# Optimization experiments

Hardware: AMD Instinct MI355X
Metric: run time of the kernel (lower is better)

## Reference

```python
import jax, jax.numpy as jnp
import numpy as np

B, S, DIM = 8, 1024, 192
D2 = 2 * DIM            # inner width 384
CH = 4                  # cell heads (= qk_size)
HD = D2 // CH           # 96 head dim
NB = D2 // 4            # 96 block-diagonal blocks
BLK = D2 // NB          # block size 4
TAU = float(HD) ** 0.5


def setup_inputs() -> dict:
    key = jax.random.key(0)
    ks = jax.random.split(key, 16)
    r = lambda i, shp, s=0.02: jax.random.normal(ks[i], shp, jnp.float32) * s
    return {
        "x": jax.random.normal(ks[0], (B, S, DIM), jnp.float32),
        "ln_g": jnp.ones((DIM,), jnp.float32), "ln_b": jnp.zeros((DIM,), jnp.float32),
        "w1": r(1, (D2, DIM)), "b1": jnp.zeros((D2,), jnp.float32),
        "w2": r(2, (D2, DIM)), "b2": jnp.zeros((D2,), jnp.float32),
        "conv_w": r(3, (D2, 1, 3), 0.1), "conv_b": jnp.zeros((D2,), jnp.float32),
        "qw": r(4, (NB, BLK, BLK), 0.1), "qb": jnp.zeros((D2,), jnp.float32),
        "kw": r(5, (NB, BLK, BLK), 0.1), "kb": jnp.zeros((D2,), jnp.float32),
        "vw": r(6, (NB, BLK, BLK), 0.1), "vb": jnp.zeros((D2,), jnp.float32),
        "wi": r(7, (CH, 3 * D2)), "bi": jax.random.normal(ks[8], (CH,), jnp.float32) * 0.1,
        "wf": r(9, (CH, 3 * D2)), "bf": jnp.linspace(3.0, 6.0, CH).astype(jnp.float32),
        "gn_g": jnp.ones((D2,), jnp.float32), "gn_b": jnp.zeros((D2,), jnp.float32),
        "wo": r(10, (DIM, D2)), "bo": jnp.zeros((DIM,), jnp.float32),
        "skip": jnp.ones((D2,), jnp.float32),
    }


def _layernorm(x, g, b):
    m = x.mean(-1, keepdims=True)
    v = ((x - m) ** 2).mean(-1, keepdims=True)
    return (x - m) / jnp.sqrt(v + 1e-5) * g + b


def _blockdiag(x, w, b):
    # x: [B,S,D2] -> blocks [B,S,NB,BLK]; w: [NB, out_blk, in_blk]
    bs, sq, _ = x.shape
    y = jnp.einsum('bsni,noi->bsno', x.reshape(bs, sq, NB, BLK), w)
    return y.reshape(bs, sq, D2) + b


def _dwconv(x, w, b):
    # depthwise conv over sequence: x [B,S,C] -> [B,C,S] conv -> [B,S,C]
    y = jax.lax.conv_general_dilated(
        x.transpose(0, 2, 1), w, window_strides=(1,), padding=[(1, 1)],
        dimension_numbers=('NCH', 'OIH', 'NCH'), feature_group_count=D2)
    return y.transpose(0, 2, 1) + b


def _cell(q, k, v, wi, bi, wf, bf, gn_g, gn_b):
    bs, sq, _ = q.shape
    gi = jnp.concatenate([q, k, v], axis=-1)                      # [B,S,3*D2]
    it = jnp.einsum('bsc,hc->bhs', gi, wi) + bi[None, :, None]    # [B,H,S]
    ft = jnp.einsum('bsc,hc->bhs', gi, wf) + bf[None, :, None]
    c = jnp.cumsum(jax.nn.log_sigmoid(ft), axis=-1)               # [B,H,S]
    logm = c[..., :, None] - c[..., None, :]                      # cum[i]-cum[j]
    mask = jnp.tril(jnp.ones((sq, sq), dtype=bool))
    f_act = jnp.where(mask, logm, -jnp.inf)
    dt = f_act + it[:, :, None, :]                                # add itilde over cols
    max_d = jnp.max(dt, axis=-1, keepdims=True)
    dmat = jnp.exp(dt - max_d)                                    # [B,H,S,S]
    qh = q.reshape(bs, sq, CH, HD).transpose(0, 2, 1, 3)
    kh = k.reshape(bs, sq, CH, HD).transpose(0, 2, 1, 3)
    vh = v.reshape(bs, sq, CH, HD).transpose(0, 2, 1, 3)
    ct = jnp.einsum('bhid,bhjd->bhij', qh, kh) * dmat / TAU
    maxit = jnp.maximum(jnp.abs(ct.sum(-1, keepdims=True)), jnp.exp(-max_d))
    h = jnp.einsum('bhij,bhjd->bhid', ct, vh) / (maxit + 1e-6)
    h = h.transpose(0, 2, 1, 3).reshape(bs, sq, CH, HD)           # per-token GroupNorm
    mu = h.mean(-1, keepdims=True)
    var = ((h - mu) ** 2).mean(-1, keepdims=True)
    h = (h - mu) / jnp.sqrt(var + 1e-5)
    h = h * gn_g.reshape(CH, HD) + gn_b.reshape(CH, HD)
    return h.reshape(bs, sq, D2)


def reference(x, ln_g, ln_b, w1, b1, w2, b2, conv_w, conv_b, qw, qb, kw, kb,
              vw, vb, wi, bi, wf, bf, gn_g, gn_b, wo, bo, skip):
    inputs = _layernorm(x, ln_g, ln_b)
    a = inputs @ w1.T + b1                   # [B,S,D2]
    bgate = jax.nn.silu(inputs @ w2.T + b2)  # [B,S,D2]
    qk = jax.nn.silu(_dwconv(a, conv_w, conv_b))
    q = _blockdiag(qk, qw, qb)
    k = _blockdiag(qk, kw, kb)
    v = _blockdiag(a, vw, vb)
    out1 = _cell(q, k, v, wi, bi, wf, bf, gn_g, gn_b)
    out1 = (out1 + skip * qk) * bgate
    out = out1 @ wo.T + bo
    return out + x
```

## Files before the change

kernel.cpp:

```cpp
#include <hip/hip_runtime.h>
#include <cstdint>

#define TAU_ 9.797958971132712f

typedef __attribute__((ext_vector_type(4))) float f32x4;
typedef __attribute__((ext_vector_type(8))) short short8;

#define DEV static __device__ __forceinline__

DEV unsigned short f2bf(float f){
  union { float f; unsigned u; } v; v.f = f;
  unsigned r = v.u + 0x7FFFu + ((v.u >> 16) & 1u);
  return (unsigned short)(r >> 16);
}
DEV float bf2f(unsigned short u){
  union { unsigned u; float f; } v; v.u = ((unsigned)u) << 16; return v.f;
}
DEV unsigned pack2bf(float a, float b){
  unsigned r;
  asm("v_cvt_pk_bf16_f32 %0, %1, %2" : "=v"(r) : "v"(a), "v"(b));
  return r;
}
DEV f32x4 ld_bf4(const unsigned short* p){
  uint2 r = *(const uint2*)p;
  f32x4 o;
  o[0] = bf2f((unsigned short)(r.x & 0xffff));
  o[1] = bf2f((unsigned short)(r.x >> 16));
  o[2] = bf2f((unsigned short)(r.y & 0xffff));
  o[3] = bf2f((unsigned short)(r.y >> 16));
  return o;
}
DEV float siluf_(float x){ return x / (1.f + __expf(-x)); }
DEV float logsigf_(float x){ return fminf(x, 0.f) - log1pf(__expf(-fabsf(x))); }

__global__ __launch_bounds__(256) void k1a_ln(
    const float* __restrict__ x, const float* __restrict__ ln_g, const float* __restrict__ ln_b,
    const float* __restrict__ w1, const float* __restrict__ w2, const float* __restrict__ wo,
    short* __restrict__ xnbf, short* __restrict__ w12bf, short* __restrict__ wobf)
{
  const int tid = threadIdx.x;
  if(blockIdx.x >= 512){
    const int idx4 = (blockIdx.x - 512) * 256 + tid;
    const float* src; short* dst; int off;
    if(idx4 < 18432)      { src = w1; dst = w12bf;         off = idx4; }
    else if(idx4 < 36864) { src = w2; dst = w12bf + 73728; off = idx4 - 18432; }
    else                  { src = wo; dst = wobf;          off = idx4 - 36864; }
    f32x4 v = *(const f32x4*)(src + off * 4);
    uint2 pk; pk.x = pack2bf(v[0], v[1]); pk.y = pack2bf(v[2], v[3]);
    *(uint2*)(dst + off * 4) = pk;
    return;
  }
  const int t = blockIdx.x * 16 + (tid >> 4);
  const int g = tid & 15;
  const float* xr = x + (long)t * 192 + g * 12;
  f32x4 v0 = *(const f32x4*)(xr);
  f32x4 v1 = *(const f32x4*)(xr + 4);
  f32x4 v2 = *(const f32x4*)(xr + 8);
  float s  = v0[0]+v0[1]+v0[2]+v0[3] + v1[0]+v1[1]+v1[2]+v1[3] + v2[0]+v2[1]+v2[2]+v2[3];
  float sq = v0[0]*v0[0]+v0[1]*v0[1]+v0[2]*v0[2]+v0[3]*v0[3]
           + v1[0]*v1[0]+v1[1]*v1[1]+v1[2]*v1[2]+v1[3]*v1[3]
           + v2[0]*v2[0]+v2[1]*v2[1]+v2[2]*v2[2]+v2[3]*v2[3];
  s  += __shfl_xor(s, 1);  s  += __shfl_xor(s, 2);  s  += __shfl_xor(s, 4);  s  += __shfl_xor(s, 8);
  sq += __shfl_xor(sq, 1); sq += __shfl_xor(sq, 2); sq += __shfl_xor(sq, 4); sq += __shfl_xor(sq, 8);
  const float mean = s * (1.f/192.f);
  const float rstd = rsqrtf(sq * (1.f/192.f) - mean * mean + 1e-5f);
  const int c0 = g * 12;
  f32x4 g0 = *(const f32x4*)(ln_g + c0),     b0 = *(const f32x4*)(ln_b + c0);
  f32x4 g1 = *(const f32x4*)(ln_g + c0 + 4), b1 = *(const f32x4*)(ln_b + c0 + 4);
  f32x4 g2 = *(const f32x4*)(ln_g + c0 + 8), b2 = *(const f32x4*)(ln_b + c0 + 8);
  unsigned pk[6];
  pk[0] = pack2bf((v0[0]-mean)*rstd*g0[0]+b0[0], (v0[1]-mean)*rstd*g0[1]+b0[1]);
  pk[1] = pack2bf((v0[2]-mean)*rstd*g0[2]+b0[2], (v0[3]-mean)*rstd*g0[3]+b0[3]);
  pk[2] = pack2bf((v1[0]-mean)*rstd*g1[0]+b1[0], (v1[1]-mean)*rstd*g1[1]+b1[1]);
  pk[3] = pack2bf((v1[2]-mean)*rstd*g1[2]+b1[2], (v1[3]-mean)*rstd*g1[3]+b1[3]);
  pk[4] = pack2bf((v2[0]-mean)*rstd*g2[0]+b2[0], (v2[1]-mean)*rstd*g2[1]+b2[1]);
  pk[5] = pack2bf((v2[2]-mean)*rstd*g2[2]+b2[2], (v2[3]-mean)*rstd*g2[3]+b2[3]);
  uint2* xo = (uint2*)(xnbf + (long)t * 192 + g * 12);
  xo[0] = make_uint2(pk[0], pk[1]);
  xo[1] = make_uint2(pk[2], pk[3]);
  xo[2] = make_uint2(pk[4], pk[5]);
}

__global__ __launch_bounds__(256) void k1b_gemm(
    const short* __restrict__ xnbf, const short* __restrict__ w12bf,
    const float* __restrict__ b1, const float* __restrict__ b2,
    unsigned short* __restrict__ abf, unsigned short* __restrict__ bgate)
{
  __shared__ short wt[18432];
  const int tid = threadIdx.x;
  const int ntg = blockIdx.x & 7;
  const int t0 = (blockIdx.x >> 3) * 128;
  {
    const short* src = w12bf + (long)ntg * 96 * 192;
    #pragma unroll
    for(int i = 0; i < 9; i++){
      const int u = i * 256 + tid;
      const int row = u / 24;
      const int dst = (u * 16) ^ ((row & 7) << 4);
      *(short8*)((char*)wt + dst) = *(const short8*)(src + u * 8);
    }
  }
  __syncthreads();
  const int widx = tid >> 6, lane = tid & 63, qg = lane >> 4, l16 = lane & 15;
  const int m0 = t0 + widx * 32;
  f32x4 acc[2][6];
  #pragma unroll
  for(int mt = 0; mt < 2; mt++)
    #pragma unroll
    for(int nt = 0; nt < 6; nt++) acc[mt][nt] = (f32x4){0.f,0.f,0.f,0.f};
  const short* xrow0 = xnbf + (long)(m0 + l16) * 192;
  const short* xrow1 = xnbf + (long)(m0 + 16 + l16) * 192;
  #pragma unroll
  for(int kc = 0; kc < 6; kc++){
    short8 af0 = *(const short8*)(xrow0 + kc * 32 + 8 * qg);
    short8 af1 = *(const short8*)(xrow1 + kc * 32 + 8 * qg);
    #pragma unroll
    for(int nt = 0; nt < 6; nt++){
      const int row = nt * 16 + l16;
      int byte = row * 384 + (kc * 32 + 8 * qg) * 2;
      byte ^= (row & 7) << 4;
      short8 bfr = *(const short8*)((const char*)wt + byte);
      acc[0][nt] = __builtin_amdgcn_mfma_f32_16x16x32_bf16(af0, bfr, acc[0][nt], 0, 0, 0);
      acc[1][nt] = __builtin_amdgcn_mfma_f32_16x16x32_bf16(af1, bfr, acc[1][nt], 0, 0, 0);
    }
  }
  const int half = ntg >> 2;
  const float* bias = half ? b2 : b1;
  const int ncol = (ntg & 3) * 96;
  #pragma unroll
  for(int mt = 0; mt < 2; mt++){
    #pragma unroll
    for(int nt = 0; nt < 6; nt++){
      const int n = ncol + nt * 16 + l16;
      const float bs = bias[n];
      #pragma unroll
      for(int r = 0; r < 4; r++){
        const int trow = m0 + mt * 16 + 4 * qg + r;
        float v = acc[mt][nt][r] + bs;
        if(half) bgate[(long)trow * 384 + n] = f2bf(siluf_(v));
        else     abf[(long)trow * 384 + n] = f2bf(v);
      }
    }
  }
}

__global__ __launch_bounds__(256) void k2bv(
    const unsigned short* __restrict__ abf,
    const float* __restrict__ cw, const float* __restrict__ cb,
    const float* __restrict__ qw, const float* __restrict__ qb,
    const float* __restrict__ kw, const float* __restrict__ kb,
    const float* __restrict__ vw, const float* __restrict__ vb,
    unsigned short* __restrict__ qkbf, short* __restrict__ qbf, short* __restrict__ kbf,
    short* __restrict__ vbf, short* __restrict__ vtbf)
{
  __shared__ float vt[64][97];
  const int tid = threadIdx.x;
  const int bh = blockIdx.x >> 4;
  const int b = bh >> 2, h = bh & 3;
  const int s0 = (blockIdx.x & 15) << 6;
  #pragma unroll
  for(int it = 0; it < 6; it++){
    const int f = it * 256 + tid;
    const int sl = f / 24, c4l = f % 24;
    const int c4 = h * 24 + c4l;
    const int s = s0 + sl;
    const long t = (long)b * 1024 + s;
    const long abase = t * 384 + c4 * 4;
    f32x4 am = ld_bf4(abf + abase);
    f32x4 al = (s > 0)    ? ld_bf4(abf + abase - 384) : (f32x4){0.f,0.f,0.f,0.f};
    f32x4 ar = (s < 1023) ? ld_bf4(abf + abase + 384) : (f32x4){0.f,0.f,0.f,0.f};
    f32x4 cw0 = *(const f32x4*)(cw + c4 * 12);
    f32x4 cw1 = *(const f32x4*)(cw + c4 * 12 + 4);
    f32x4 cw2 = *(const f32x4*)(cw + c4 * 12 + 8);
    f32x4 cb4 = *(const f32x4*)(cb + c4 * 4);
    f32x4 in;
    in[0] = siluf_(cb4[0] + al[0]*cw0[0] + am[0]*cw0[1] + ar[0]*cw0[2]);
    in[1] = siluf_(cb4[1] + al[1]*cw0[3] + am[1]*cw1[0] + ar[1]*cw1[1]);
    in[2] = siluf_(cb4[2] + al[2]*cw1[2] + am[2]*cw1[3] + ar[2]*cw2[0]);
    in[3] = siluf_(cb4[3] + al[3]*cw2[1] + am[3]*cw2[2] + ar[3]*cw2[3]);
    {
      uint2 pk; pk.x = pack2bf(in[0], in[1]); pk.y = pack2bf(in[2], in[3]);
      *(uint2*)(qkbf + abase) = pk;
    }
    const long base = ((long)(b * 4 + h) * 1024 + s) * 96 + c4l * 4;
    {
      const float* w = qw + c4 * 16;
      float v0 = qb[c4*4+0] + w[0]*in[0]  + w[1]*in[1]  + w[2]*in[2]  + w[3]*in[3];
      float v1 = qb[c4*4+1] + w[4]*in[0]  + w[5]*in[1]  + w[6]*in[2]  + w[7]*in[3];
      float v2 = qb[c4*4+2] + w[8]*in[0]  + w[9]*in[1]  + w[10]*in[2] + w[11]*in[3];
      float v3 = qb[c4*4+3] + w[12]*in[0] + w[13]*in[1] + w[14]*in[2] + w[15]*in[3];
      uint2 pk; pk.x = pack2bf(v0, v1); pk.y = pack2bf(v2, v3);
      *(uint2*)(qbf + base) = pk;
    }
    {
      const float* w = kw + c4 * 16;
      float v0 = kb[c4*4+0] + w[0]*in[0]  + w[1]*in[1]  + w[2]*in[2]  + w[3]*in[3];
      float v1 = kb[c4*4+1] + w[4]*in[0]  + w[5]*in[1]  + w[6]*in[2]  + w[7]*in[3];
      float v2 = kb[c4*4+2] + w[8]*in[0]  + w[9]*in[1]  + w[10]*in[2] + w[11]*in[3];
      float v3 = kb[c4*4+3] + w[12]*in[0] + w[13]*in[1] + w[14]*in[2] + w[15]*in[3];
      uint2 pk; pk.x = pack2bf(v0, v1); pk.y = pack2bf(v2, v3);
      *(uint2*)(kbf + base) = pk;
    }
    {
      const float* w = vw + c4 * 16;
      float vv[4];
      #pragma unroll
      for(int o = 0; o < 4; o++){
        float v = vb[c4*4+o] + w[o*4]*am[0] + w[o*4+1]*am[1] + w[o*4+2]*am[2] + w[o*4+3]*am[3];
        vv[o] = v;
        vt[sl][c4l * 4 + o] = v;
      }
      uint2 pk; pk.x = pack2bf(vv[0], vv[1]); pk.y = pack2bf(vv[2], vv[3]);
      *(uint2*)(vbf + abase) = pk;
    }
  }
  __syncthreads();
  #pragma unroll
  for(int it = 0; it < 24; it++){
    const int f = it * 256 + tid;
    const int d = f >> 6, sl = f & 63;
    vtbf[((long)bh * 96 + d) * 1024 + s0 + sl] = (short)f2bf(vt[sl][d]);
  }
}

__global__ __launch_bounds__(256) void k2c_gates(
    const short* __restrict__ qbf, const short* __restrict__ kbf, const short* __restrict__ vbf,
    const float* __restrict__ wi, const float* __restrict__ bi,
    const float* __restrict__ wf, const float* __restrict__ bff,
    float* __restrict__ itv, float* __restrict__ ftv)
{
  __shared__ short wg[8 * 1160];
  const int tid = threadIdx.x;
  const int t0 = blockIdx.x * 64;
  #pragma unroll
  for(int i = 0; i < 9; i++){
    const int u = i * 256 + tid;
    const int row = u / 288, col4 = u % 288;
    const float* src = ((row < 4) ? wi + row * 1152 : wf + (row - 4) * 1152) + col4 * 4;
    f32x4 v = *(const f32x4*)src;
    uint2 pk; pk.x = pack2bf(v[0], v[1]); pk.y = pack2bf(v[2], v[3]);
    *(uint2*)(&wg[row * 1160 + col4 * 4]) = pk;
  }
  __syncthreads();
  const int w = tid >> 6, lane = tid & 63, qg = lane >> 4, l16 = lane & 15;
  const int tw = t0 + w * 16;
  const int tA = tw + l16;
  const int b = tA >> 10, s = tA & 1023;
  f32x4 acc = (f32x4){0.f,0.f,0.f,0.f};
  #pragma unroll
  for(int kc = 0; kc < 36; kc++){
    const int blk = kc / 3;
    const int off = (kc % 3) * 32 + qg * 8;
    short8 af;
    if(blk < 4)      af = *(const short8*)(qbf + ((long)(b*4+blk)*1024 + s)*96 + off);
    else if(blk < 8) af = *(const short8*)(kbf + ((long)(b*4+blk-4)*1024 + s)*96 + off);
    else             af = *(const short8*)(vbf + (long)tA*384 + (blk-8)*96 + off);
    short8 bf8 = *(const short8*)(&wg[(l16 & 7) * 1160 + kc * 32 + qg * 8]);
    acc = __builtin_amdgcn_mfma_f32_16x16x32_bf16(af, bf8, acc, 0, 0, 0);
  }
  if(l16 < 8){
    const int gh = l16 & 3;
    const float bias = (l16 < 4) ? bi[gh] : bff[gh];
    float* dst = (l16 < 4) ? itv : ftv;
    #pragma unroll
    for(int r = 0; r < 4; r++){
      const int t = tw + 4 * qg + r;
      dst[((long)((t >> 10) * 4 + gh)) * 1024 + (t & 1023)] = acc[r] + bias;
    }
  }
}

__global__ __launch_bounds__(256) void k3_scan(
    const float* __restrict__ itv, const float* __restrict__ ftv,
    float* __restrict__ Ev, float* __restrict__ Rpv, float* __restrict__ dsv)
{
  __shared__ float sb[256];
  const int bh = blockIdx.x, tid = threadIdx.x;
  const long base = (long)bh * 1024 + tid * 4;
  f32x4 f4 = *(const f32x4*)(ftv + base);
  const float l0 = logsigf_(f4[0]);
  const float l1 = logsigf_(f4[1]);
  const float l2 = logsigf_(f4[2]);
  const float l3 = logsigf_(f4[3]);
  float c0 = l0, c1 = l0 + l1, c2 = c1 + l2, c3 = c2 + l3;
  sb[tid] = c3;
  __syncthreads();
  for(int off = 1; off < 256; off <<= 1){
    float mine = sb[tid];
    float oth = (tid >= off) ? sb[tid - off] : 0.f;
    __syncthreads();
    sb[tid] = mine + oth;
    __syncthreads();
  }
  const float excl = (tid > 0) ? sb[tid - 1] : 0.f;
  c0 += excl; c1 += excl; c2 += excl; c3 += excl;
  f32x4 i4 = *(const f32x4*)(itv + base);
  const float m0 = i4[0] - c0, m1 = i4[1] - c1, m2 = i4[2] - c2, m3 = i4[3] - c3;
  const float x1 = fmaxf(m0, m1), x2 = fmaxf(x1, m2), x3 = fmaxf(x2, m3);
  __syncthreads();
  sb[tid] = x3;
  __syncthreads();
  for(int off = 1; off < 256; off <<= 1){
    float mine = sb[tid];
    float oth = (tid >= off) ? sb[tid - off] : -3.4e38f;
    __syncthreads();
    sb[tid] = fmaxf(mine, oth);
    __syncthreads();
  }
  const float exm = (tid > 0) ? sb[tid - 1] : -3.4e38f;
  const float M0 = fmaxf(m0, exm);
  const float M1 = fmaxf(x1, exm);
  const float M2 = fmaxf(x2, exm);
  const float M3 = fmaxf(x3, exm);
  f32x4 e, rp, ds;
  e[0] = __expf(m0); e[1] = __expf(m1); e[2] = __expf(m2); e[3] = __expf(m3);
  rp[0] = __expf(-M0) * (1.f/TAU_); rp[1] = __expf(-M1) * (1.f/TAU_);
  rp[2] = __expf(-M2) * (1.f/TAU_); rp[3] = __expf(-M3) * (1.f/TAU_);
  ds[0] = __expf(-(c0 + M0)); ds[1] = __expf(-(c1 + M1));
  ds[2] = __expf(-(c2 + M2)); ds[3] = __expf(-(c3 + M3));
  *(f32x4*)(Ev  + base) = e;
  *(f32x4*)(Rpv + base) = rp;
  *(f32x4*)(dsv + base) = ds;
}

__global__ __launch_bounds__(256, 2) void k4_attn(
    const short* __restrict__ qbf, const short* __restrict__ kbf, const short* __restrict__ vtbf,
    const float* __restrict__ Ev, const float* __restrict__ Rpv, const float* __restrict__ dsv,
    const float* __restrict__ gn_g, const float* __restrict__ gn_b,
    const unsigned short* __restrict__ qkbf, const unsigned short* __restrict__ bgate,
    const float* __restrict__ skip, short* __restrict__ o1bf)
{
  __shared__ short kbuf[2][64 * 104];
  __shared__ short vbuf[2][96 * 72];
  __shared__ float ebuf[2][64];
  __shared__ short P[4][16][72];
  const int tid = threadIdx.x;
  const int w = tid >> 6, lane = tid & 63, qg = lane >> 4, l16 = lane & 15;
  const int xcd = blockIdx.x & 7, q = blockIdx.x >> 3;
  const int bh = ((q & 3) << 3) | xcd;
  const int qh = q >> 2;
  const int ib = (q < 32) ? (15 - qh) : (qh - 8);
  const int i0w = ib * 64 + w * 16;
  const long qkbase = (long)bh * 1024;
  const int nj = ib + 1;

  short8 qf[3];
  #pragma unroll
  for(int kc = 0; kc < 3; kc++)
    qf[kc] = *(const short8*)(qbf + (qkbase + i0w + l16) * 96 + kc * 32 + 8 * qg);
  const float rp = Rpv[qkbase + i0w + l16];
  const float ds = dsv[qkbase + i0w + l16];

  f32x4 acc[6];
  #pragma unroll
  for(int dt = 0; dt < 6; dt++) acc[dt] = (f32x4){0.f,0.f,0.f,0.f};
  float bp = 0.f;

  const int rK0 = tid / 12,        cK0 = tid % 12;
  const int rK1 = (tid+256) / 12,  cK1 = (tid+256) % 12;
  const int rK2 = (tid+512) / 12,  cK2 = (tid+512) % 12;
  const int dV0 = tid >> 3,        cV0 = tid & 7;
  const int dV1 = (tid+256) >> 3,  cV1 = (tid+256) & 7;
  const int dV2 = (tid+512) >> 3,  cV2 = (tid+512) & 7;
  const bool he = (tid < 16);
  short8 sk0, sk1, sk2, sv0, sv1, sv2; f32x4 se;
  const short* kgb = kbf + qkbase * 96;
  const short* vgb = vtbf + (long)bh * 96 * 1024;

#define STAGE_LOAD(J0)                                              \
  {                                                                 \
    const int j0_ = (J0);                                           \
    sk0 = *(const short8*)(kgb + (j0_ + rK0) * 96 + cK0 * 8);       \
    sk1 = *(const short8*)(kgb + (j0_ + rK1) * 96 + cK1 * 8);       \
    sk2 = *(const short8*)(kgb + (j0_ + rK2) * 96 + cK2 * 8);       \
    sv0 = *(const short8*)(vgb + (long)dV0 * 1024 + j0_ + cV0 * 8); \
    sv1 = *(const short8*)(vgb + (long)dV1 * 1024 + j0_ + cV1 * 8); \
    sv2 = *(const short8*)(vgb + (long)dV2 * 1024 + j0_ + cV2 * 8); \
    if(he) se = *(const f32x4*)(Ev + qkbase + j0_ + tid * 4);       \
  }

#define STAGE_WRITE(B)                                   \
  {                                                      \
    *(short8*)(&kbuf[B][rK0 * 104 + cK0 * 8]) = sk0;     \
    *(short8*)(&kbuf[B][rK1 * 104 + cK1 * 8]) = sk1;     \
    *(short8*)(&kbuf[B][rK2 * 104 + cK2 * 8]) = sk2;     \
    *(short8*)(&vbuf[B][dV0 * 72 + cV0 * 8]) = sv0;      \
    *(short8*)(&vbuf[B][dV1 * 72 + cV1 * 8]) = sv1;      \
    *(short8*)(&vbuf[B][dV2 * 72 + cV2 * 8]) = sv2;      \
    if(he) *(f32x4*)(&ebuf[B][tid * 4]) = se;            \
  }

  STAGE_LOAD(0);
  int cur = 0;
  for(int jt = 0; jt < nj; jt++){
    STAGE_WRITE(cur);
    __syncthreads();
    if(jt + 1 < nj) STAGE_LOAD((jt + 1) * 64);

    const int j0 = jt * 64;
    const bool diag = (jt == nj - 1);
    const int i = i0w + l16;
    __builtin_amdgcn_s_setprio(1);
    #pragma unroll
    for(int jsub = 0; jsub < 4; jsub++){
      f32x4 C = (f32x4){0.f,0.f,0.f,0.f};
      #pragma unroll
      for(int kc = 0; kc < 3; kc++){
        short8 kf = *(const short8*)(&kbuf[cur][(jsub*16 + l16) * 104 + kc * 32 + 8 * qg]);
        C = __builtin_amdgcn_mfma_f32_16x16x32_bf16(kf, qf[kc], C, 0, 0, 0);
      }
      f32x4 e4 = *(const f32x4*)(&ebuf[cur][jsub * 16 + 4 * qg]);
      float v0 = C[0] * e4[0];
      float v1 = C[1] * e4[1];
      float v2 = C[2] * e4[2];
      float v3 = C[3] * e4[3];
      if(diag){
        const int jb = j0 + jsub * 16 + 4 * qg;
        if(jb + 0 > i) v0 = 0.f;
        if(jb + 1 > i) v1 = 0.f;
        if(jb + 2 > i) v2 = 0.f;
        if(jb + 3 > i) v3 = 0.f;
      }
      bp += v0 + v1 + v2 + v3;
      uint2 pw; pw.x = pack2bf(v0, v1); pw.y = pack2bf(v2, v3);
      *(uint2*)(&P[w][l16][jsub * 16 + 4 * qg]) = pw;
    }
    asm volatile("s_waitcnt lgkmcnt(0)" ::: "memory");
    #pragma unroll
    for(int ksub = 0; ksub < 2; ksub++){
      short8 pa = *(const short8*)(&P[w][l16][ksub * 32 + 8 * qg]);
      #pragma unroll
      for(int dt = 0; dt < 6; dt++){
        short8 vf = *(const short8*)(&vbuf[cur][(dt * 16 + l16) * 72 + ksub * 32 + 8 * qg]);
        acc[dt] = __builtin_amdgcn_mfma_f32_16x16x32_bf16(pa, vf, acc[dt], 0, 0, 0);
      }
    }
    __builtin_amdgcn_s_setprio(0);
    cur ^= 1;
  }
#undef STAGE_LOAD
#undef STAGE_WRITE

  const int head = bh & 3, bb = bh >> 2;
  short8 q8v[3], g8v[3];
  f32x4 s0v[3], s1v[3];
  long offv[3];
  #pragma unroll
  for(int u2 = 0; u2 < 3; u2++){
    const int f = u2 * 256 + tid;
    const int row = f / 12, c8 = f % 12;
    const long off = ((long)(bb * 1024 + ib * 64 + row)) * 384 + head * 96 + c8 * 8;
    offv[u2] = off;
    q8v[u2] = *(const short8*)((const short*)qkbf + off);
    g8v[u2] = *(const short8*)((const short*)bgate + off);
    s0v[u2] = *(const f32x4*)(skip + head * 96 + c8 * 8);
    s1v[u2] = *(const f32x4*)(skip + head * 96 + c8 * 8 + 4);
  }

  float bsum = bp;
  bsum += __shfl_xor(bsum, 16);
  bsum += __shfl_xor(bsum, 32);
  const float bfull = bsum * rp;
  const float den = fmaxf(fabsf(bfull), ds) + 1e-6f;
  const float sc = rp / den;
  float srow[4];
  #pragma unroll
  for(int r = 0; r < 4; r++) srow[r] = __shfl(sc, 4 * qg + r);
  float hv[6][4], mu[4], rs[4];
  #pragma unroll
  for(int r = 0; r < 4; r++){
    float sm = 0.f, sq = 0.f;
    #pragma unroll
    for(int dt = 0; dt < 6; dt++){
      const float h = acc[dt][r] * srow[r];
      hv[dt][r] = h; sm += h; sq += h * h;
    }
    sm += __shfl_xor(sm, 1); sm += __shfl_xor(sm, 2); sm += __shfl_xor(sm, 4); sm += __shfl_xor(sm, 8);
    sq += __shfl_xor(sq, 1); sq += __shfl_xor(sq, 2); sq += __shfl_xor(sq, 4); sq += __shfl_xor(sq, 8);
    const float m_ = sm * (1.f/96.f);
    mu[r] = m_;
    rs[r] = rsqrtf(sq * (1.f/96.f) - m_ * m_ + 1e-5f);
  }
  __syncthreads();
  short* hstage = &kbuf[0][0];
  #pragma unroll
  for(int dt = 0; dt < 6; dt++){
    const int col = head * 96 + dt * 16 + l16;
    const float g  = gn_g[col];
    const float be = gn_b[col];
    #pragma unroll
    for(int r = 0; r < 4; r++){
      const float hn = (hv[dt][r] - mu[r]) * rs[r] * g + be;
      hstage[(w * 16 + 4 * qg + r) * 104 + dt * 16 + l16] = (short)f2bf(hn);
    }
  }
  __syncthreads();
  #pragma unroll
  for(int u2 = 0; u2 < 3; u2++){
    const int f = u2 * 256 + tid;
    const int row = f / 12, c8 = f % 12;
    short8 h8 = *(const short8*)(hstage + row * 104 + c8 * 8);
    short8 q8 = q8v[u2];
    short8 g8 = g8v[u2];
    float o[8];
    #pragma unroll
    for(int i = 0; i < 8; i++){
      const float sk = (i < 4) ? s0v[u2][i] : s1v[u2][i - 4];
      o[i] = (bf2f((unsigned short)h8[i]) + sk * bf2f((unsigned short)q8[i]))
             * bf2f((unsigned short)g8[i]);
    }
    union { short8 s; unsigned u4[4]; } ov;
    ov.u4[0] = pack2bf(o[0], o[1]); ov.u4[1] = pack2bf(o[2], o[3]);
    ov.u4[2] = pack2bf(o[4], o[5]); ov.u4[3] = pack2bf(o[6], o[7]);
    *(short8*)(o1bf + offv[u2]) = ov.s;
  }
}

__global__ __launch_bounds__(256) void k5_gemm(
    const short* __restrict__ o1bf, const short* __restrict__ wobf,
    const float* __restrict__ bo, const float* __restrict__ x, float* __restrict__ out)
{
  __shared__ short wt[18432];
  const int tid = threadIdx.x;
  const int ng = blockIdx.x & 3;
  const int t0 = (blockIdx.x >> 2) * 128;
  {
    const short* src = wobf + (long)ng * 48 * 384;
    #pragma unroll
    for(int i = 0; i < 9; i++){
      const int u = i * 256 + tid;
      const int row = u / 48;
      const int dst = (u * 16) ^ ((row & 7) << 4);
      *(short8*)((char*)wt + dst) = *(const short8*)(src + u * 8);
    }
  }
  __syncthreads();
  const int widx = tid >> 6, lane = tid & 63, qg = lane >> 4, l16 = lane & 15;
  const int m0 = t0 + widx * 32;
  f32x4 acc[2][3];
  #pragma unroll
  for(int mt = 0; mt < 2; mt++)
    #pragma unroll
    for(int nt = 0; nt < 3; nt++) acc[mt][nt] = (f32x4){0.f,0.f,0.f,0.f};
  const short* arow0 = o1bf + (long)(m0 + l16) * 384;
  const short* arow1 = o1bf + (long)(m0 + 16 + l16) * 384;
  #pragma unroll
  for(int kc = 0; kc < 12; kc++){
    short8 af0 = *(const short8*)(arow0 + kc * 32 + 8 * qg);
    short8 af1 = *(const short8*)(arow1 + kc * 32 + 8 * qg);
    #pragma unroll
    for(int nt = 0; nt < 3; nt++){
      const int row = nt * 16 + l16;
      int byte = row * 768 + kc * 64 + qg * 16;
      byte ^= (row & 7) << 4;
      short8 bfr = *(const short8*)((const char*)wt + byte);
      acc[0][nt] = __builtin_amdgcn_mfma_f32_16x16x32_bf16(af0, bfr, acc[0][nt], 0, 0, 0);
      acc[1][nt] = __builtin_amdgcn_mfma_f32_16x16x32_bf16(af1, bfr, acc[1][nt], 0, 0, 0);
    }
  }
  #pragma unroll
  for(int mt = 0; mt < 2; mt++){
    #pragma unroll
    for(int nt = 0; nt < 3; nt++){
      const int n = ng * 48 + nt * 16 + l16;
      const float b_ = bo[n];
      #pragma unroll
      for(int r = 0; r < 4; r++){
        const int trow = m0 + mt * 16 + 4 * qg + r;
        out[(long)trow * 192 + n] = acc[mt][nt][r] + b_ + x[(long)trow * 192 + n];
      }
    }
  }
}

extern "C" void kernel_launch(void* const* d_in, const int* in_sizes, int n_in,
                              void* d_out, int out_size, void* d_ws, size_t ws_size,
                              hipStream_t stream)
{
  (void)in_sizes; (void)n_in; (void)out_size; (void)ws_size;
  const float* x    = (const float*)d_in[0];
  const float* ln_g = (const float*)d_in[1];
  const float* ln_b = (const float*)d_in[2];
  const float* w1   = (const float*)d_in[3];
  const float* b1   = (const float*)d_in[4];
  const float* w2   = (const float*)d_in[5];
  const float* b2   = (const float*)d_in[6];
  const float* cw   = (const float*)d_in[7];
  const float* cb   = (const float*)d_in[8];
  const float* qw   = (const float*)d_in[9];
  const float* qb   = (const float*)d_in[10];
  const float* kw   = (const float*)d_in[11];
  const float* kb   = (const float*)d_in[12];
  const float* vw   = (const float*)d_in[13];
  const float* vb   = (const float*)d_in[14];
  const float* wi   = (const float*)d_in[15];
  const float* bi   = (const float*)d_in[16];
  const float* wf   = (const float*)d_in[17];
  const float* bff  = (const float*)d_in[18];
  const float* gn_g = (const float*)d_in[19];
  const float* gn_b = (const float*)d_in[20];
  const float* wo   = (const float*)d_in[21];
  const float* bo   = (const float*)d_in[22];
  const float* skip = (const float*)d_in[23];
  float* out = (float*)d_out;

  char* ws = (char*)d_ws;
  unsigned short* abf   = (unsigned short*)(ws + 0);
  short* vbf   = (short*)(ws + 6291456);
  unsigned short* bgate = (unsigned short*)(ws + 12582912);
  unsigned short* qkbf  = (unsigned short*)(ws + 25165824);
  short* xnbf  = (short*)(ws + 37748736);
  short* w12bf = (short*)(ws + 40894464);
  short* wobf  = (short*)(ws + 41189376);
  short* o1bf  = (short*)(ws + 41943040);
  short* qbf   = (short*)(ws + 50331648);
  short* kbf   = (short*)(ws + 56623104);
  short* vtbf  = (short*)(ws + 62914560);
  float* itv   = (float*)(ws + 69648384);
  float* ftv   = (float*)(ws + 69779456);
  float* Ev    = (float*)(ws + 69910528);
  float* Rpv   = (float*)(ws + 70041600);
  float* dsv   = (float*)(ws + 70172672);

  k1a_ln<<<728, 256, 0, stream>>>(x, ln_g, ln_b, w1, w2, wo, xnbf, w12bf, wobf);
  k1b_gemm<<<512, 256, 0, stream>>>(xnbf, w12bf, b1, b2, abf, bgate);
  k2bv<<<512, 256, 0, stream>>>(abf, cw, cb, qw, qb, kw, kb, vw, vb, qkbf, qbf, kbf, vbf, vtbf);
  k2c_gates<<<128, 256, 0, stream>>>(qbf, kbf, vbf, wi, bi, wf, bff, itv, ftv);
  k3_scan<<<32, 256, 0, stream>>>(itv, ftv, Ev, Rpv, dsv);
  k4_attn<<<512, 256, 0, stream>>>(qbf, kbf, vtbf, Ev, Rpv, dsv, gn_g, gn_b,
                                   qkbf, bgate, skip, o1bf);
  k5_gemm<<<256, 256, 0, stream>>>(o1bf, wobf, bo, x, out);
}
```

Baseline: 78.81 us.

## Fuse gate prefix-scan into attention kernel, recomputing per block

Removes the separate scan kernel launch and its global round-trip for the exp/stabilizer arrays. Each attention block now recomputes the full 1024-length log-sigmoid prefix sum and running-max scan for its (batch, head) in shared memory, keeping all E values resident and extracting its own 64 rows of rp/ds. This trades one launch and intermediate traffic for redundant scan work, with 16 blocks repeating the same scan and about 16 extra barriers, plus roughly 5 KB more LDS per block, which may affect occupancy.

```diff
diff --git a/kernel.cpp b/kernel.cpp
--- a/kernel.cpp
+++ b/kernel.cpp
@@ -270,70 +270,19 @@
   }
 }
 
-__global__ __launch_bounds__(256) void k3_scan(
-    const float* __restrict__ itv, const float* __restrict__ ftv,
-    float* __restrict__ Ev, float* __restrict__ Rpv, float* __restrict__ dsv)
-{
-  __shared__ float sb[256];
-  const int bh = blockIdx.x, tid = threadIdx.x;
-  const long base = (long)bh * 1024 + tid * 4;
-  f32x4 f4 = *(const f32x4*)(ftv + base);
-  const float l0 = logsigf_(f4[0]);
-  const float l1 = logsigf_(f4[1]);
-  const float l2 = logsigf_(f4[2]);
-  const float l3 = logsigf_(f4[3]);
-  float c0 = l0, c1 = l0 + l1, c2 = c1 + l2, c3 = c2 + l3;
-  sb[tid] = c3;
-  __syncthreads();
-  for(int off = 1; off < 256; off <<= 1){
-    float mine = sb[tid];
-    float oth = (tid >= off) ? sb[tid - off] : 0.f;
-    __syncthreads();
-    sb[tid] = mine + oth;
-    __syncthreads();
-  }
-  const float excl = (tid > 0) ? sb[tid - 1] : 0.f;
-  c0 += excl; c1 += excl; c2 += excl; c3 += excl;
-  f32x4 i4 = *(const f32x4*)(itv + base);
-  const float m0 = i4[0] - c0, m1 = i4[1] - c1, m2 = i4[2] - c2, m3 = i4[3] - c3;
-  const float x1 = fmaxf(m0, m1), x2 = fmaxf(x1, m2), x3 = fmaxf(x2, m3);
-  __syncthreads();
-  sb[tid] = x3;
-  __syncthreads();
-  for(int off = 1; off < 256; off <<= 1){
-    float mine = sb[tid];
-    float oth = (tid >= off) ? sb[tid - off] : -3.4e38f;
-    __syncthreads();
-    sb[tid] = fmaxf(mine, oth);
-    __syncthreads();
-  }
-  const float exm = (tid > 0) ? sb[tid - 1] : -3.4e38f;
-  const float M0 = fmaxf(m0, exm);
-  const float M1 = fmaxf(x1, exm);
-  const float M2 = fmaxf(x2, exm);
-  const float M3 = fmaxf(x3, exm);
-  f32x4 e, rp, ds;
-  e[0] = __expf(m0); e[1] = __expf(m1); e[2] = __expf(m2); e[3] = __expf(m3);
-  rp[0] = __expf(-M0) * (1.f/TAU_); rp[1] = __expf(-M1) * (1.f/TAU_);
-  rp[2] = __expf(-M2) * (1.f/TAU_); rp[3] = __expf(-M3) * (1.f/TAU_);
-  ds[0] = __expf(-(c0 + M0)); ds[1] = __expf(-(c1 + M1));
-  ds[2] = __expf(-(c2 + M2)); ds[3] = __expf(-(c3 + M3));
-  *(f32x4*)(Ev  + base) = e;
-  *(f32x4*)(Rpv + base) = rp;
-  *(f32x4*)(dsv + base) = ds;
-}
-
 __global__ __launch_bounds__(256, 2) void k4_attn(
     const short* __restrict__ qbf, const short* __restrict__ kbf, const short* __restrict__ vtbf,
-    const float* __restrict__ Ev, const float* __restrict__ Rpv, const float* __restrict__ dsv,
+    const float* __restrict__ itv, const float* __restrict__ ftv,
     const float* __restrict__ gn_g, const float* __restrict__ gn_b,
     const unsigned short* __restrict__ qkbf, const unsigned short* __restrict__ bgate,
     const float* __restrict__ skip, short* __restrict__ o1bf)
 {
   __shared__ short kbuf[2][64 * 104];
   __shared__ short vbuf[2][96 * 72];
-  __shared__ float ebuf[2][64];
   __shared__ short P[4][16][72];
+  __shared__ float eall[1024];
+  __shared__ float rpL[64], dsL[64];
+  __shared__ float sb[256];
   const int tid = threadIdx.x;
   const int w = tid >> 6, lane = tid & 63, qg = lane >> 4, l16 = lane & 15;
   const int xcd = blockIdx.x & 7, q = blockIdx.x >> 3;
@@ -344,26 +293,13 @@
   const long qkbase = (long)bh * 1024;
   const int nj = ib + 1;
 
-  short8 qf[3];
-  #pragma unroll
-  for(int kc = 0; kc < 3; kc++)
-    qf[kc] = *(const short8*)(qbf + (qkbase + i0w + l16) * 96 + kc * 32 + 8 * qg);
-  const float rp = Rpv[qkbase + i0w + l16];
-  const float ds = dsv[qkbase + i0w + l16];
-
-  f32x4 acc[6];
-  #pragma unroll
-  for(int dt = 0; dt < 6; dt++) acc[dt] = (f32x4){0.f,0.f,0.f,0.f};
-  float bp = 0.f;
-
   const int rK0 = tid / 12,        cK0 = tid % 12;
   const int rK1 = (tid+256) / 12,  cK1 = (tid+256) % 12;
   const int rK2 = (tid+512) / 12,  cK2 = (tid+512) % 12;
   const int dV0 = tid >> 3,        cV0 = tid & 7;
   const int dV1 = (tid+256) >> 3,  cV1 = (tid+256) & 7;
   const int dV2 = (tid+512) >> 3,  cV2 = (tid+512) & 7;
-  const bool he = (tid < 16);
-  short8 sk0, sk1, sk2, sv0, sv1, sv2; f32x4 se;
+  short8 sk0, sk1, sk2, sv0, sv1, sv2;
   const short* kgb = kbf + qkbase * 96;
   const short* vgb = vtbf + (long)bh * 96 * 1024;
 
@@ -376,7 +312,6 @@
     sv0 = *(const short8*)(vgb + (long)dV0 * 1024 + j0_ + cV0 * 8); \
     sv1 = *(const short8*)(vgb + (long)dV1 * 1024 + j0_ + cV1 * 8); \
     sv2 = *(const short8*)(vgb + (long)dV2 * 1024 + j0_ + cV2 * 8); \
-    if(he) se = *(const f32x4*)(Ev + qkbase + j0_ + tid * 4);       \
   }
 
 #define STAGE_WRITE(B)                                   \
@@ -387,10 +322,75 @@
     *(short8*)(&vbuf[B][dV0 * 72 + cV0 * 8]) = sv0;      \
     *(short8*)(&vbuf[B][dV1 * 72 + cV1 * 8]) = sv1;      \
     *(short8*)(&vbuf[B][dV2 * 72 + cV2 * 8]) = sv2;      \
-    if(he) *(f32x4*)(&ebuf[B][tid * 4]) = se;            \
   }
 
   STAGE_LOAD(0);
+  short8 qf[3];
+  #pragma unroll
+  for(int kc = 0; kc < 3; kc++)
+    qf[kc] = *(const short8*)(qbf + (qkbase + i0w + l16) * 96 + kc * 32 + 8 * qg);
+
+  {
+    const long sbase = qkbase + tid * 4;
+    f32x4 f4 = *(const f32x4*)(ftv + sbase);
+    const float l0 = logsigf_(f4[0]);
+    const float l1 = logsigf_(f4[1]);
+    const float l2 = logsigf_(f4[2]);
+    const float l3 = logsigf_(f4[3]);
+    float c0 = l0, c1 = l0 + l1, c2 = c1 + l2, c3 = c2 + l3;
+    sb[tid] = c3;
+    __syncthreads();
+    for(int off = 1; off < 256; off <<= 1){
+      float mine = sb[tid];
+      float oth = (tid >= off) ? sb[tid - off] : 0.f;
+      __syncthreads();
+      sb[tid] = mine + oth;
+      __syncthreads();
+    }
+    const float excl = (tid > 0) ? sb[tid - 1] : 0.f;
+    c0 += excl; c1 += excl; c2 += excl; c3 += excl;
+    f32x4 i4 = *(const f32x4*)(itv + sbase);
+    const float m0 = i4[0] - c0, m1 = i4[1] - c1, m2 = i4[2] - c2, m3 = i4[3] - c3;
+    const float x1 = fmaxf(m0, m1), x2 = fmaxf(x1, m2), x3 = fmaxf(x2, m3);
+    __syncthreads();
+    sb[tid] = x3;
+    __syncthreads();
+    for(int off = 1; off < 256; off <<= 1){
+      float mine = sb[tid];
+      float oth = (tid >= off) ? sb[tid - off] : -3.4e38f;
+      __syncthreads();
+      sb[tid] = fmaxf(mine, oth);
+      __syncthreads();
+    }
+    const float exm = (tid > 0) ? sb[tid - 1] : -3.4e38f;
+    const float M0 = fmaxf(m0, exm);
+    const float M1 = fmaxf(x1, exm);
+    const float M2 = fmaxf(x2, exm);
+    const float M3 = fmaxf(x3, exm);
+    f32x4 ev;
+    ev[0] = __expf(m0); ev[1] = __expf(m1); ev[2] = __expf(m2); ev[3] = __expf(m3);
+    *(f32x4*)(&eall[tid * 4]) = ev;
+    float rpv4[4], dsv4[4];
+    rpv4[0] = __expf(-M0) * (1.f/TAU_); rpv4[1] = __expf(-M1) * (1.f/TAU_);
+    rpv4[2] = __expf(-M2) * (1.f/TAU_); rpv4[3] = __expf(-M3) * (1.f/TAU_);
+    dsv4[0] = __expf(-(c0 + M0)); dsv4[1] = __expf(-(c1 + M1));
+    dsv4[2] = __expf(-(c2 + M2)); dsv4[3] = __expf(-(c3 + M3));
+    const int p0 = tid * 4;
+    #pragma unroll
+    for(int e = 0; e < 4; e++){
+      const int rel = p0 + e - ib * 64;
+      if(rel >= 0 && rel < 64){ rpL[rel] = rpv4[e]; dsL[rel] = dsv4[e]; }
+    }
+    __syncthreads();
+  }
+  const float rp = rpL[w * 16 + l16];
+  const float ds = dsL[w * 16 + l16];
+
+  f32x4 acc[6];
+  #pragma unroll
+  for(int dt = 0; dt < 6; dt++) acc[dt] = (f32x4){0.f,0.f,0.f,0.f};
+  float bp = 0.f;
+
   int cur = 0;
   for(int jt = 0; jt < nj; jt++){
     STAGE_WRITE(cur);
@@ -409,7 +409,7 @@
         short8 kf = *(const short8*)(&kbuf[cur][(jsub*16 + l16) * 104 + kc * 32 + 8 * qg]);
         C = __builtin_amdgcn_mfma_f32_16x16x32_bf16(kf, qf[kc], C, 0, 0, 0);
       }
-      f32x4 e4 = *(const f32x4*)(&ebuf[cur][jsub * 16 + 4 * qg]);
+      f32x4 e4 = *(const f32x4*)(&eall[j0 + jsub * 16 + 4 * qg]);
       float v0 = C[0] * e4[0];
       float v1 = C[1] * e4[1];
       float v2 = C[2] * e4[2];
@@ -618,16 +618,12 @@
   short* vtbf  = (short*)(ws + 62914560);
   float* itv   = (float*)(ws + 69648384);
   float* ftv   = (float*)(ws + 69779456);
-  float* Ev    = (float*)(ws + 69910528);
-  float* Rpv   = (float*)(ws + 70041600);
-  float* dsv   = (float*)(ws + 70172672);
 
   k1a_ln<<<728, 256, 0, stream>>>(x, ln_g, ln_b, w1, w2, wo, xnbf, w12bf, wobf);
   k1b_gemm<<<512, 256, 0, stream>>>(xnbf, w12bf, b1, b2, abf, bgate);
   k2bv<<<512, 256, 0, stream>>>(abf, cw, cb, qw, qb, kw, kb, vw, vb, qkbf, qbf, kbf, vbf, vtbf);
   k2c_gates<<<128, 256, 0, stream>>>(qbf, kbf, vbf, wi, bi, wf, bff, itv, ftv);
-  k3_scan<<<32, 256, 0, stream>>>(itv, ftv, Ev, Rpv, dsv);
-  k4_attn<<<512, 256, 0, stream>>>(qbf, kbf, vtbf, Ev, Rpv, dsv, gn_g, gn_b,
+  k4_attn<<<512, 256, 0, stream>>>(qbf, kbf, vtbf, itv, ftv, gn_g, gn_b,
                                    qkbf, bgate, skip, o1bf);
   k5_gemm<<<256, 256, 0, stream>>>(o1bf, wobf, bo, x, out);
 }
```

After: 75.33 us. 1.05x faster.
